# Kernel optimization log

Hardware: AMD Instinct MI355X
Metric: run time of the kernel (lower is better)

Reference implementation:

```python
import jax, jax.numpy as jnp
import numpy as np

C = 256
HEADS = 8
HEAD_DIM = C // HEADS
GROUPS = 8
EPS = 1e-5


def setup_inputs() -> dict:
    key = jax.random.key(0)
    ks = jax.random.split(key, 11)
    B, S = 2, 16
    s = 0.02
    return {
        "x": jax.random.normal(ks[0], (B, C, S, S, S), dtype=jnp.float32),
        "gn_w": jnp.ones((C,), jnp.float32),
        "gn_b": jnp.zeros((C,), jnp.float32),
        "wq": jax.random.normal(ks[1], (C, C), jnp.float32) * s,
        "bq": jnp.zeros((C,), jnp.float32),
        "wk": jax.random.normal(ks[2], (C, C), jnp.float32) * s,
        "bk": jnp.zeros((C,), jnp.float32),
        "wv": jax.random.normal(ks[3], (C, C), jnp.float32) * s,
        "bv": jnp.zeros((C,), jnp.float32),
        "wo": jax.random.normal(ks[4], (C, C), jnp.float32) * s,
        "bo": jnp.zeros((C,), jnp.float32),
    }


def _group_norm(x, w, b):
    # x: [B, C, D, H, W]; GroupNorm(8, C) with affine params
    B, Cc, D, H, W = x.shape
    xg = x.reshape(B, GROUPS, Cc // GROUPS, D, H, W)
    mu = jnp.mean(xg, axis=(2, 3, 4, 5), keepdims=True)
    var = jnp.mean(jnp.square(xg - mu), axis=(2, 3, 4, 5), keepdims=True)
    xn = ((xg - mu) * jax.lax.rsqrt(var + EPS)).reshape(B, Cc, D, H, W)
    return xn * w[None, :, None, None, None] + b[None, :, None, None, None]


def reference(x, gn_w, gn_b, wq, bq, wk, bk, wv, bv, wo, bo):
    B, Cc, D, H, W = x.shape
    N = D * H * W
    xn = _group_norm(x, gn_w, gn_b).reshape(B, Cc, N)  # [B,C,N]
    # 1x1x1 Conv3d == per-voxel linear: weight [out,in]
    Q = jnp.einsum("oc,bcn->bon", wq, xn) + bq[None, :, None]
    K = jnp.einsum("oc,bcn->bon", wk, xn) + bk[None, :, None]
    V = jnp.einsum("oc,bcn->bon", wv, xn) + bv[None, :, None]
    Q = Q.reshape(B, HEADS, HEAD_DIM, N)
    K = K.reshape(B, HEADS, HEAD_DIM, N)
    V = V.reshape(B, HEADS, HEAD_DIM, N)
    scale = np.sqrt(HEAD_DIM).astype(np.float32)
    attn = jnp.einsum("bhdn,bhdm->bhnm", Q, K) / scale
    attn = jax.nn.softmax(attn, axis=-1)
    out = jnp.einsum("bhnm,bhdm->bhdn", attn, V)  # [B,h,hd,N]
    out = out.reshape(B, Cc, N)
    out = jnp.einsum("oc,bcn->bon", wo, out) + bo[None, :, None]
    return x + out.reshape(B, Cc, D, H, W)
```

## Files before the change

### kernel.cpp

```cpp
#include <hip/hip_runtime.h>

#define B_   2
#define C_   256
#define N_   4096
#define H_   8
#define HD_  32
#define G_   8
#define CPG_ 32

typedef short short8 __attribute__((ext_vector_type(8)));
typedef float f32x4  __attribute__((ext_vector_type(4)));
typedef float f4     __attribute__((ext_vector_type(4)));

__device__ __forceinline__ float b2f(short s) {
    return __uint_as_float(((unsigned)(unsigned short)s) << 16);
}
__device__ __forceinline__ short f2b(float f) {
    unsigned u = __float_as_uint(f);
    unsigned r = (u + 0x7FFF + ((u >> 16) & 1)) >> 16;
    return (short)r;
}

__global__ __launch_bounds__(256) void gn_part(const float* __restrict__ x,
                                               float* __restrict__ part) {
    int blk = blockIdx.x;
    const f4* p = (const f4*)x + (size_t)(blk >> 6) * (CPG_ * N_ / 4) + (size_t)(blk & 63) * 512;
    float s = 0.f, ss = 0.f;
#pragma unroll
    for (int i = 0; i < 2; i++) {
        f4 v = p[threadIdx.x + i * 256];
#pragma unroll
        for (int j = 0; j < 4; j++) { float f = v[j]; s += f; ss += f * f; }
    }
#pragma unroll
    for (int off = 32; off > 0; off >>= 1) {
        s  += __shfl_down(s, off);
        ss += __shfl_down(ss, off);
    }
    __shared__ float rs[4], rss[4];
    int w = threadIdx.x >> 6;
    if ((threadIdx.x & 63) == 0) { rs[w] = s; rss[w] = ss; }
    __syncthreads();
    if (threadIdx.x == 0) {
        part[blk * 2]     = rs[0] + rs[1] + rs[2] + rs[3];
        part[blk * 2 + 1] = rss[0] + rss[1] + rss[2] + rss[3];
    }
}

__global__ __launch_bounds__(256) void gemm_qkv(
    const float* __restrict__ x,
    const float* __restrict__ gw, const float* __restrict__ gb,
    const float* __restrict__ part,
    const float* __restrict__ wq, const float* __restrict__ bq,
    const float* __restrict__ wk, const float* __restrict__ bk,
    const float* __restrict__ wv, const float* __restrict__ bv,
    short* __restrict__ q, short* __restrict__ kt, short* __restrict__ v) {
    int z = blockIdx.z;
    int b = z / 3, which = z % 3;
    const float* W    = which == 0 ? wq : (which == 1 ? wk : wv);
    const float* bias = which == 0 ? bq : (which == 1 ? bk : bv);
    bool trans = (which != 2);
    float mul = (which == 0) ? (0.17677669529663687f * 1.4426950408889634f) : 1.0f;

    __shared__ short wl[64][40];
    __shared__ short xl[128][40];
    __shared__ float ga[256], gbb[256];
    __shared__ float mus[8], rstds[8];

    int o0 = blockIdx.y * 64, n0 = blockIdx.x * 128;
    int tid = threadIdx.x;
    int w = tid >> 6, lane = tid & 63, li = lane & 15, quad = lane >> 4;
    int wr = w & 1, wc = w >> 1;

#pragma unroll
    for (int gi = 0; gi < 2; gi++) {
        int g = w * 2 + gi;
        const float* pp = &part[(size_t)(b * 8 + g) * 128 + lane * 2];
        float s = pp[0], ss = pp[1];
#pragma unroll
        for (int off = 32; off > 0; off >>= 1) {
            s  += __shfl_down(s, off);
            ss += __shfl_down(ss, off);
        }
        if (lane == 0) {
            const float inv = 1.f / (float)(CPG_ * N_);
            float mu = s * inv;
            float var = ss * inv - mu * mu;
            mus[g] = mu;
            rstds[g] = rsqrtf(var + 1e-5f);
        }
    }
    __syncthreads();
    {
        int c = tid, g = c >> 5;
        float a = rstds[g] * gw[c];
        ga[c]  = a;
        gbb[c] = gb[c] - mus[g] * a;
    }

    f32x4 acc[8];
#pragma unroll
    for (int i = 0; i < 8; i++) acc[i] = (f32x4){0.f, 0.f, 0.f, 0.f};

    int cpair = tid >> 4, l16 = tid & 15;
    __syncthreads();

    for (int k0 = 0; k0 < 256; k0 += 32) {
        {
            int row = tid >> 2, co = (tid & 3) << 3;
            const float* wp = &W[(size_t)(o0 + row) * 256 + k0 + co];
            f4 wa = *(const f4*)wp;
            f4 wb = *(const f4*)(wp + 4);
            short8 w8;
#pragma unroll
            for (int j = 0; j < 4; j++) { w8[j] = f2b(wa[j]); w8[j + 4] = f2b(wb[j]); }
            *(short8*)&wl[row][co] = w8;
        }
        {
            int c0 = k0 + cpair * 2;
            float a0 = ga[c0],     b0c = gbb[c0];
            float a1 = ga[c0 + 1], b1c = gbb[c0 + 1];
            const float* xr0 = x + ((size_t)(b * 256 + c0)) * N_ + n0 + l16;
            const float* xr1 = xr0 + N_;
#pragma unroll
            for (int j = 0; j < 8; j++) {
                unsigned lo = (unsigned short)f2b(xr0[16 * j] * a0 + b0c);
                unsigned hi = (unsigned short)f2b(xr1[16 * j] * a1 + b1c);
                *(unsigned*)&xl[l16 + 16 * j][cpair * 2] = lo | (hi << 16);
            }
        }
        __syncthreads();
        short8 af[4], bfr[4];
        if (trans) {
#pragma unroll
            for (int i = 0; i < 4; i++) af[i]  = *(short8*)&xl[wr * 64 + i * 16 + li][quad * 8];
#pragma unroll
            for (int j = 0; j < 2; j++) bfr[j] = *(short8*)&wl[wc * 32 + j * 16 + li][quad * 8];
#pragma unroll
            for (int i = 0; i < 4; i++)
#pragma unroll
                for (int j = 0; j < 2; j++)
                    acc[i * 2 + j] = __builtin_amdgcn_mfma_f32_16x16x32_bf16(af[i], bfr[j], acc[i * 2 + j], 0, 0, 0);
        } else {
#pragma unroll
            for (int i = 0; i < 2; i++) af[i]  = *(short8*)&wl[wr * 32 + i * 16 + li][quad * 8];
#pragma unroll
            for (int j = 0; j < 4; j++) bfr[j] = *(short8*)&xl[wc * 64 + j * 16 + li][quad * 8];
#pragma unroll
            for (int i = 0; i < 2; i++)
#pragma unroll
                for (int j = 0; j < 4; j++)
                    acc[i * 4 + j] = __builtin_amdgcn_mfma_f32_16x16x32_bf16(af[i], bfr[j], acc[i * 4 + j], 0, 0, 0);
        }
        __syncthreads();
    }

    if (which == 2) {
        short* outp = v + (size_t)b * C_ * N_;
#pragma unroll
        for (int i = 0; i < 2; i++) {
            int ob = o0 + wr * 32 + i * 16 + quad * 4;
#pragma unroll
            for (int j = 0; j < 4; j++) {
                int n_ = n0 + wc * 64 + j * 16 + li;
#pragma unroll
                for (int r = 0; r < 4; r++) {
                    float val = acc[i * 4 + j][r] + bias[ob + r];
                    outp[(size_t)(ob + r) * N_ + n_] = f2b(val);
                }
            }
        }
    } else if (which == 0) {
        short* outp = q + (size_t)b * N_ * C_;
#pragma unroll
        for (int i = 0; i < 4; i++) {
            int nb_ = n0 + wr * 64 + i * 16 + quad * 4;
#pragma unroll
            for (int j = 0; j < 2; j++) {
                int o_ = o0 + wc * 32 + j * 16 + li;
                float bv_ = bias[o_];
#pragma unroll
                for (int r = 0; r < 4; r++)
                    outp[(size_t)(nb_ + r) * C_ + o_] = f2b((acc[i * 2 + j][r] + bv_) * mul);
            }
        }
    } else {
#pragma unroll
        for (int i = 0; i < 4; i++) {
            int nb_ = n0 + wr * 64 + i * 16 + quad * 4;
#pragma unroll
            for (int j = 0; j < 2; j++) {
                int o_ = o0 + wc * 32 + j * 16 + li;
                int hh = o_ >> 5, d = o_ & 31;
                float bv_ = bias[o_];
                short* kdst = kt + ((size_t)(b * 8 + hh) * N_) * HD_ + d;
#pragma unroll
                for (int r = 0; r < 4; r++)
                    kdst[(size_t)(nb_ + r) * HD_] = f2b(acc[i * 2 + j][r] + bv_);
            }
        }
    }
}

#define STAGE_BARRIER(bufk, bufv)                                         \
    *(short8*)&kl[(bufk) * 2560 + klo] = kst;                             \
    *(short8*)&vl[(bufv) * 2304 + vlo] = vst;                             \
    __syncthreads();

#define PREFETCH(t1)                                                      \
    kst = *(const short8*)(kgp + (size_t)(t1) * 64 * HD_);                \
    vst = *(const short8*)(vgp + (t1) * 64);

#define LOADVF(vf, bufv)                                                  \
    vf[0] = *(short8*)&vl[(bufv) * 2304 + li * 72 + quad * 8];            \
    vf[1] = *(short8*)&vl[(bufv) * 2304 + (16 + li) * 72 + quad * 8];     \
    vf[2] = *(short8*)&vl[(bufv) * 2304 + li * 72 + 32 + quad * 8];       \
    vf[3] = *(short8*)&vl[(bufv) * 2304 + (16 + li) * 72 + 32 + quad * 8];

#define QK(bufk)                                                          \
    _Pragma("unroll")                                                     \
    for (int c = 0; c < 4; c++) {                                         \
        short8 kf = *(short8*)&kl[(bufk) * 2560 + (c * 16 + li) * 40 + quad * 8]; \
        s0[c] = __builtin_amdgcn_mfma_f32_16x16x32_bf16(kf, qf0, zero, 0, 0, 0);  \
        s1[c] = __builtin_amdgcn_mfma_f32_16x16x32_bf16(kf, qf1, zero, 0, 0, 0);  \
    }

#define PV(pP, vf)                                                        \
    {                                                                     \
        short8 pf00 = *(short8*)&(pP)[li * 72 + quad * 8];                \
        short8 pf01 = *(short8*)&(pP)[li * 72 + 32 + quad * 8];           \
        short8 pf10 = *(short8*)&(pP)[1152 + li * 72 + quad * 8];         \
        short8 pf11 = *(short8*)&(pP)[1152 + li * 72 + 32 + quad * 8];    \
        oa00 = __builtin_amdgcn_mfma_f32_16x16x32_bf16(pf00, vf[0], oa00, 0, 0, 0); \
        oa01 = __builtin_amdgcn_mfma_f32_16x16x32_bf16(pf00, vf[1], oa01, 0, 0, 0); \
        oa00 = __builtin_amdgcn_mfma_f32_16x16x32_bf16(pf01, vf[2], oa00, 0, 0, 0); \
        oa01 = __builtin_amdgcn_mfma_f32_16x16x32_bf16(pf01, vf[3], oa01, 0, 0, 0); \
        oa10 = __builtin_amdgcn_mfma_f32_16x16x32_bf16(pf10, vf[0], oa10, 0, 0, 0); \
        oa11 = __builtin_amdgcn_mfma_f32_16x16x32_bf16(pf10, vf[1], oa11, 0, 0, 0); \
        oa10 = __builtin_amdgcn_mfma_f32_16x16x32_bf16(pf11, vf[2], oa10, 0, 0, 0); \
        oa11 = __builtin_amdgcn_mfma_f32_16x16x32_bf16(pf11, vf[3], oa11, 0, 0, 0); \
    }

#define EXPPACK(pC)                                                       \
    {                                                                     \
        float lp = 0.f;                                                   \
        _Pragma("unroll")                                                 \
        for (int c = 0; c < 4; c++) {                                     \
            float e0 = __builtin_amdgcn_exp2f(s0[c][0]);                  \
            float e1 = __builtin_amdgcn_exp2f(s0[c][1]);                  \
            float e2 = __builtin_amdgcn_exp2f(s0[c][2]);                  \
            float e3 = __builtin_amdgcn_exp2f(s0[c][3]);                  \
            lp += (e0 + e1) + (e2 + e3);                                  \
            unsigned pk0 = __builtin_amdgcn_perm(__float_as_uint(e1), __float_as_uint(e0), 0x07060302); \
            unsigned pk1 = __builtin_amdgcn_perm(__float_as_uint(e3), __float_as_uint(e2), 0x07060302); \
            uint2 pkv; pkv.x = pk0; pkv.y = pk1;                          \
            *(uint2*)&(pC)[li * 72 + c * 16 + quad * 4] = pkv;            \
        }                                                                 \
        lr0 += lp;                                                        \
        lp = 0.f;                                                         \
        _Pragma("unroll")                                                 \
        for (int c = 0; c < 4; c++) {                                     \
            float e0 = __builtin_amdgcn_exp2f(s1[c][0]);                  \
            float e1 = __builtin_amdgcn_exp2f(s1[c][1]);                  \
            float e2 = __builtin_amdgcn_exp2f(s1[c][2]);                  \
            float e3 = __builtin_amdgcn_exp2f(s1[c][3]);                  \
            lp += (e0 + e1) + (e2 + e3);                                  \
            unsigned pk0 = __builtin_amdgcn_perm(__float_as_uint(e1), __float_as_uint(e0), 0x07060302); \
            unsigned pk1 = __builtin_amdgcn_perm(__float_as_uint(e3), __float_as_uint(e2), 0x07060302); \
            uint2 pkv; pkv.x = pk0; pkv.y = pk1;                          \
            *(uint2*)&(pC)[1152 + li * 72 + c * 16 + quad * 4] = pkv;     \
        }                                                                 \
        lr1 += lp;                                                        \
    }

__global__ __launch_bounds__(256) void flash(const short* __restrict__ q,
                                             const short* __restrict__ ktp,
                                             const short* __restrict__ v,
                                             short* __restrict__ aoT) {
    int bid = blockIdx.x;
    int xcd = bid & 7;
    int s_  = bid >> 3;
    int bh  = xcd * 2 + (s_ & 1);
    int nb  = s_ >> 1;
    int b = bh >> 3, h = bh & 7;

    const short* QT = q   + (size_t)b * N_ * C_ + h * HD_;
    const short* KP = ktp + (size_t)bh * N_ * HD_;
    const short* V  = v   + ((size_t)b * C_ + h * HD_) * N_;
    short* O = aoT + (size_t)b * N_ * C_ + h * HD_;

    __shared__ short kl[2 * 2560];
    __shared__ short vl[2 * 2304];
    __shared__ short pl[4 * 4608];

    int tid = threadIdx.x, w = tid >> 6, lane = tid & 63, li = lane & 15, quad = lane >> 4;
    int n0w = nb * 128 + w * 32;
    short* pA = pl + w * 4608;
    short* pB = pA + 2304;

    short8 qf0 = *(const short8*)&QT[(size_t)(n0w + li) * 256 + quad * 8];
    short8 qf1 = *(const short8*)&QT[(size_t)(n0w + 16 + li) * 256 + quad * 8];

    f32x4 oa00 = (f32x4){0.f,0.f,0.f,0.f}, oa01 = oa00, oa10 = oa00, oa11 = oa00;
    float lr0 = 0.f, lr1 = 0.f;
    const f32x4 zero = (f32x4){0.f, 0.f, 0.f, 0.f};

    int krow = tid >> 2, kcol = (tid & 3) << 3;
    int vrow = tid >> 3, vcol = (tid & 7) << 3;
    const short* kgp = KP + (size_t)krow * HD_ + kcol;
    const short* vgp = V + (size_t)vrow * N_ + vcol;
    int klo = krow * 40 + kcol;
    int vlo = vrow * 72 + vcol;

    short8 kst = *(const short8*)kgp;
    short8 vst = *(const short8*)vgp;
    short8 vfa[4], vfb[4];
    f32x4 s0[4], s1[4];

    STAGE_BARRIER(0, 0);
    PREFETCH(1);
    LOADVF(vfa, 0);
    QK(0);
    EXPPACK(pA);

    for (int mt = 1; mt < 62; mt += 2) {
        STAGE_BARRIER(1, 1);
        PREFETCH(mt + 1);
        LOADVF(vfb, 1);
        QK(1);
        PV(pA, vfa);
        EXPPACK(pB);
        STAGE_BARRIER(0, 0);
        PREFETCH(mt + 2);
        LOADVF(vfa, 0);
        QK(0);
        PV(pB, vfb);
        EXPPACK(pA);
    }
    STAGE_BARRIER(1, 1);
    LOADVF(vfb, 1);
    QK(1);
    PV(pA, vfa);
    EXPPACK(pB);
    PV(pB, vfb);

    lr0 += __shfl_xor(lr0, 16); lr0 += __shfl_xor(lr0, 32);
    lr1 += __shfl_xor(lr1, 16); lr1 += __shfl_xor(lr1, 32);
#pragma unroll
    for (int r2 = 0; r2 < 4; r2++) {
        float ln0 = __shfl(lr0, quad * 4 + r2);
        float inv0 = 1.f / ln0;
        size_t n_ = (size_t)(n0w + quad * 4 + r2);
        O[n_ * 256 + li]      = f2b(oa00[r2] * inv0);
        O[n_ * 256 + 16 + li] = f2b(oa01[r2] * inv0);
        float ln1 = __shfl(lr1, quad * 4 + r2);
        float inv1 = 1.f / ln1;
        size_t n2 = (size_t)(n0w + 16 + quad * 4 + r2);
        O[n2 * 256 + li]      = f2b(oa10[r2] * inv1);
        O[n2 * 256 + 16 + li] = f2b(oa11[r2] * inv1);
    }
}

__global__ __launch_bounds__(256) void gemm_out(const float* __restrict__ W,
                                                const float* __restrict__ bias,
                                                const short* __restrict__ aoT,
                                                const float* __restrict__ resid,
                                                float* __restrict__ out) {
    int b = blockIdx.z;
    const short* X = aoT + (size_t)b * N_ * C_;
    const float* R = resid + (size_t)b * C_ * N_;
    float* outp = out + (size_t)b * C_ * N_;

    __shared__ short wl[128][40];
    __shared__ short xl[64][40];

    int o0 = blockIdx.y * 128, n0 = blockIdx.x * 64;
    int tid = threadIdx.x;
    int w = tid >> 6, lane = tid & 63, li = lane & 15, quad = lane >> 4;
    int wr = w & 1, wc = w >> 1;

    f32x4 acc[4][2];
#pragma unroll
    for (int i = 0; i < 4; i++)
#pragma unroll
        for (int j = 0; j < 2; j++) acc[i][j] = (f32x4){0.f, 0.f, 0.f, 0.f};

    for (int k0 = 0; k0 < 256; k0 += 32) {
#pragma unroll
        for (int i = 0; i < 2; i++) {
            int idx = tid + i * 256;
            int row = idx >> 2, co = (idx & 3) << 3;
            const float* wp = &W[(size_t)(o0 + row) * 256 + k0 + co];
            f4 wa = *(const f4*)wp;
            f4 wb = *(const f4*)(wp + 4);
            short8 w8;
#pragma unroll
            for (int j = 0; j < 4; j++) { w8[j] = f2b(wa[j]); w8[j + 4] = f2b(wb[j]); }
            *(short8*)&wl[row][co] = w8;
        }
        {
            int row = tid >> 2, co = (tid & 3) << 3;
            *(short8*)&xl[row][co] = *(const short8*)&X[(size_t)(n0 + row) * 256 + k0 + co];
        }
        __syncthreads();
        short8 af[4], bfr[2];
#pragma unroll
        for (int i = 0; i < 4; i++) af[i]  = *(short8*)&wl[wr * 64 + i * 16 + li][quad * 8];
#pragma unroll
        for (int j = 0; j < 2; j++) bfr[j] = *(short8*)&xl[wc * 32 + j * 16 + li][quad * 8];
#pragma unroll
        for (int i = 0; i < 4; i++)
#pragma unroll
            for (int j = 0; j < 2; j++)
                acc[i][j] = __builtin_amdgcn_mfma_f32_16x16x32_bf16(af[i], bfr[j], acc[i][j], 0, 0, 0);
        __syncthreads();
    }
#pragma unroll
    for (int i = 0; i < 4; i++) {
        int ob = o0 + wr * 64 + i * 16 + quad * 4;
#pragma unroll
        for (int j = 0; j < 2; j++) {
            int n_ = n0 + wc * 32 + j * 16 + li;
#pragma unroll
            for (int r = 0; r < 4; r++) {
                size_t idx = (size_t)(ob + r) * N_ + n_;
                outp[idx] = acc[i][j][r] + bias[ob + r] + R[idx];
            }
        }
    }
}

extern "C" void kernel_launch(void* const* d_in, const int* in_sizes, int n_in,
                              void* d_out, int out_size, void* d_ws, size_t ws_size,
                              hipStream_t stream) {
    const float* x  = (const float*)d_in[0];
    const float* gw = (const float*)d_in[1];
    const float* gb = (const float*)d_in[2];
    const float* wq = (const float*)d_in[3];
    const float* bq = (const float*)d_in[4];
    const float* wk = (const float*)d_in[5];
    const float* bk = (const float*)d_in[6];
    const float* wv = (const float*)d_in[7];
    const float* bv = (const float*)d_in[8];
    const float* wo = (const float*)d_in[9];
    const float* bo = (const float*)d_in[10];
    float* out = (float*)d_out;

    char* ws = (char*)d_ws;
    float* part = (float*)ws;
    const size_t TS = (size_t)B_ * N_ * C_;
    short* aoT = (short*)(ws + 16384);
    short* q   = aoT + TS;
    short* kt  = q + TS;
    short* v   = kt + TS;

    gn_part<<<1024, 256, 0, stream>>>(x, part);
    gemm_qkv<<<dim3(32, 4, 6), 256, 0, stream>>>(x, gw, gb, part,
                                                 wq, bq, wk, bk, wv, bv, q, kt, v);
    flash<<<512, 256, 0, stream>>>(q, kt, v, aoT);
    gemm_out<<<dim3(64, 2, 2), 256, 0, stream>>>(wo, bo, aoT, x, out);
}
```

Before: 171.8 us.

## Keep softmax probabilities in registers and use 8 waves of 16 query rows

The flash kernel now runs 8 waves per block, each handling 16 query rows instead of 32. Exponentiated scores are packed straight into MFMA A-operand registers rather than written to and re-read from a shared-memory P buffer. The V tile is loaded with a permuted column order so the register layout of P matches the V fragment layout. It also adds s_setprio around the MFMA blocks and replaces the manually software-pipelined unrolled loop with a simple double-buffered loop. The aim is to remove the LDS round trip for P and raise occupancy, at the cost of more K/V LDS reads per query row and less explicit overlap.

```diff
diff --git a/kernel.cpp b/kernel.cpp
--- a/kernel.cpp
+++ b/kernel.cpp
@@ -9,6 +9,8 @@
 #define CPG_ 32
 
 typedef short short8 __attribute__((ext_vector_type(8)));
+typedef short short4v __attribute__((ext_vector_type(4)));
+typedef unsigned uint4v __attribute__((ext_vector_type(4)));
 typedef float f32x4  __attribute__((ext_vector_type(4)));
 typedef float f4     __attribute__((ext_vector_type(4)));
 
@@ -202,78 +204,7 @@
     }
 }
 
-#define STAGE_BARRIER(bufk, bufv)                                         \
-    *(short8*)&kl[(bufk) * 2560 + klo] = kst;                             \
-    *(short8*)&vl[(bufv) * 2304 + vlo] = vst;                             \
-    __syncthreads();
-
-#define PREFETCH(t1)                                                      \
-    kst = *(const short8*)(kgp + (size_t)(t1) * 64 * HD_);                \
-    vst = *(const short8*)(vgp + (t1) * 64);
-
-#define LOADVF(vf, bufv)                                                  \
-    vf[0] = *(short8*)&vl[(bufv) * 2304 + li * 72 + quad * 8];            \
-    vf[1] = *(short8*)&vl[(bufv) * 2304 + (16 + li) * 72 + quad * 8];     \
-    vf[2] = *(short8*)&vl[(bufv) * 2304 + li * 72 + 32 + quad * 8];       \
-    vf[3] = *(short8*)&vl[(bufv) * 2304 + (16 + li) * 72 + 32 + quad * 8];
-
-#define QK(bufk)                                                          \
-    _Pragma("unroll")                                                     \
-    for (int c = 0; c < 4; c++) {                                         \
-        short8 kf = *(short8*)&kl[(bufk) * 2560 + (c * 16 + li) * 40 + quad * 8]; \
-        s0[c] = __builtin_amdgcn_mfma_f32_16x16x32_bf16(kf, qf0, zero, 0, 0, 0);  \
-        s1[c] = __builtin_amdgcn_mfma_f32_16x16x32_bf16(kf, qf1, zero, 0, 0, 0);  \
-    }
-
-#define PV(pP, vf)                                                        \
-    {                                                                     \
-        short8 pf00 = *(short8*)&(pP)[li * 72 + quad * 8];                \
-        short8 pf01 = *(short8*)&(pP)[li * 72 + 32 + quad * 8];           \
-        short8 pf10 = *(short8*)&(pP)[1152 + li * 72 + quad * 8];         \
-        short8 pf11 = *(short8*)&(pP)[1152 + li * 72 + 32 + quad * 8];    \
-        oa00 = __builtin_amdgcn_mfma_f32_16x16x32_bf16(pf00, vf[0], oa00, 0, 0, 0); \
-        oa01 = __builtin_amdgcn_mfma_f32_16x16x32_bf16(pf00, vf[1], oa01, 0, 0, 0); \
-        oa00 = __builtin_amdgcn_mfma_f32_16x16x32_bf16(pf01, vf[2], oa00, 0, 0, 0); \
-        oa01 = __builtin_amdgcn_mfma_f32_16x16x32_bf16(pf01, vf[3], oa01, 0, 0, 0); \
-        oa10 = __builtin_amdgcn_mfma_f32_16x16x32_bf16(pf10, vf[0], oa10, 0, 0, 0); \
-        oa11 = __builtin_amdgcn_mfma_f32_16x16x32_bf16(pf10, vf[1], oa11, 0, 0, 0); \
-        oa10 = __builtin_amdgcn_mfma_f32_16x16x32_bf16(pf11, vf[2], oa10, 0, 0, 0); \
-        oa11 = __builtin_amdgcn_mfma_f32_16x16x32_bf16(pf11, vf[3], oa11, 0, 0, 0); \
-    }
-
-#define EXPPACK(pC)                                                       \
-    {                                                                     \
-        float lp = 0.f;                                                   \
-        _Pragma("unroll")                                                 \
-        for (int c = 0; c < 4; c++) {                                     \
-            float e0 = __builtin_amdgcn_exp2f(s0[c][0]);                  \
-            float e1 = __builtin_amdgcn_exp2f(s0[c][1]);                  \
-            float e2 = __builtin_amdgcn_exp2f(s0[c][2]);                  \
-            float e3 = __builtin_amdgcn_exp2f(s0[c][3]);                  \
-            lp += (e0 + e1) + (e2 + e3);                                  \
-            unsigned pk0 = __builtin_amdgcn_perm(__float_as_uint(e1), __float_as_uint(e0), 0x07060302); \
-            unsigned pk1 = __builtin_amdgcn_perm(__float_as_uint(e3), __float_as_uint(e2), 0x07060302); \
-            uint2 pkv; pkv.x = pk0; pkv.y = pk1;                          \
-            *(uint2*)&(pC)[li * 72 + c * 16 + quad * 4] = pkv;            \
-        }                                                                 \
-        lr0 += lp;                                                        \
-        lp = 0.f;                                                         \
-        _Pragma("unroll")                                                 \
-        for (int c = 0; c < 4; c++) {                                     \
-            float e0 = __builtin_amdgcn_exp2f(s1[c][0]);                  \
-            float e1 = __builtin_amdgcn_exp2f(s1[c][1]);                  \
-            float e2 = __builtin_amdgcn_exp2f(s1[c][2]);                  \
-            float e3 = __builtin_amdgcn_exp2f(s1[c][3]);                  \
-            lp += (e0 + e1) + (e2 + e3);                                  \
-            unsigned pk0 = __builtin_amdgcn_perm(__float_as_uint(e1), __float_as_uint(e0), 0x07060302); \
-            unsigned pk1 = __builtin_amdgcn_perm(__float_as_uint(e3), __float_as_uint(e2), 0x07060302); \
-            uint2 pkv; pkv.x = pk0; pkv.y = pk1;                          \
-            *(uint2*)&(pC)[1152 + li * 72 + c * 16 + quad * 4] = pkv;     \
-        }                                                                 \
-        lr1 += lp;                                                        \
-    }
-
-__global__ __launch_bounds__(256) void flash(const short* __restrict__ q,
+__global__ __launch_bounds__(512) void flash(const short* __restrict__ q,
                                              const short* __restrict__ ktp,
                                              const short* __restrict__ v,
                                              short* __restrict__ aoT) {
@@ -291,61 +222,80 @@
 
     __shared__ short kl[2 * 2560];
     __shared__ short vl[2 * 2304];
-    __shared__ short pl[4 * 4608];
 
     int tid = threadIdx.x, w = tid >> 6, lane = tid & 63, li = lane & 15, quad = lane >> 4;
-    int n0w = nb * 128 + w * 32;
-    short* pA = pl + w * 4608;
-    short* pB = pA + 2304;
+    int n0w = nb * 128 + w * 16;
 
     short8 qf0 = *(const short8*)&QT[(size_t)(n0w + li) * 256 + quad * 8];
-    short8 qf1 = *(const short8*)&QT[(size_t)(n0w + 16 + li) * 256 + quad * 8];
-
-    f32x4 oa00 = (f32x4){0.f,0.f,0.f,0.f}, oa01 = oa00, oa10 = oa00, oa11 = oa00;
-    float lr0 = 0.f, lr1 = 0.f;
+
+    f32x4 oa00 = (f32x4){0.f,0.f,0.f,0.f}, oa01 = oa00;
+    float lr0 = 0.f;
     const f32x4 zero = (f32x4){0.f, 0.f, 0.f, 0.f};
 
-    int krow = tid >> 2, kcol = (tid & 3) << 3;
-    int vrow = tid >> 3, vcol = (tid & 7) << 3;
+    int krow = tid >> 3, kcol = (tid & 7) << 2;
     const short* kgp = KP + (size_t)krow * HD_ + kcol;
-    const short* vgp = V + (size_t)vrow * N_ + vcol;
     int klo = krow * 40 + kcol;
-    int vlo = vrow * 72 + vcol;
-
-    short8 kst = *(const short8*)kgp;
-    short8 vst = *(const short8*)vgp;
-    short8 vfa[4], vfb[4];
-    f32x4 s0[4], s1[4];
-
-    STAGE_BARRIER(0, 0);
-    PREFETCH(1);
-    LOADVF(vfa, 0);
-    QK(0);
-    EXPPACK(pA);
-
-    for (int mt = 1; mt < 62; mt += 2) {
-        STAGE_BARRIER(1, 1);
-        PREFETCH(mt + 1);
-        LOADVF(vfb, 1);
-        QK(1);
-        PV(pA, vfa);
-        EXPPACK(pB);
-        STAGE_BARRIER(0, 0);
-        PREFETCH(mt + 2);
-        LOADVF(vfa, 0);
-        QK(0);
-        PV(pB, vfb);
-        EXPPACK(pA);
-    }
-    STAGE_BARRIER(1, 1);
-    LOADVF(vfb, 1);
-    QK(1);
-    PV(pA, vfa);
-    EXPPACK(pB);
-    PV(pB, vfb);
+    int vd = tid >> 4, g = tid & 15;
+    int mbase = 32 * (g >> 3) + 16 * (g & 1) + 4 * ((g >> 1) & 3);
+    const short* vgp = V + (size_t)vd * N_ + mbase;
+    int vlo = vd * 72 + g * 4;
+
+    short4v kst = *(const short4v*)kgp;
+    short4v vst = *(const short4v*)vgp;
+
+    f32x4 s0[4];
+    short8 vf[4];
+
+    for (int t = 0; t < 64; ++t) {
+        int buf = t & 1;
+        *(short4v*)&kl[buf * 2560 + klo] = kst;
+        *(short4v*)&vl[buf * 2304 + vlo] = vst;
+        if (t < 63) {
+            kst = *(const short4v*)(kgp + (size_t)(t + 1) * 64 * HD_);
+            vst = *(const short4v*)(vgp + (t + 1) * 64);
+        }
+        __syncthreads();
+
+        __builtin_amdgcn_s_setprio(1);
+#pragma unroll
+        for (int c = 0; c < 4; c++) {
+            short8 kf = *(short8*)&kl[buf * 2560 + (c * 16 + li) * 40 + quad * 8];
+            s0[c] = __builtin_amdgcn_mfma_f32_16x16x32_bf16(kf, qf0, zero, 0, 0, 0);
+        }
+        __builtin_amdgcn_s_setprio(0);
+
+        vf[0] = *(short8*)&vl[buf * 2304 + li * 72 + quad * 8];
+        vf[1] = *(short8*)&vl[buf * 2304 + (16 + li) * 72 + quad * 8];
+        vf[2] = *(short8*)&vl[buf * 2304 + li * 72 + 32 + quad * 8];
+        vf[3] = *(short8*)&vl[buf * 2304 + (16 + li) * 72 + 32 + quad * 8];
+
+        unsigned paw[8];
+        float lp = 0.f;
+#pragma unroll
+        for (int c = 0; c < 4; c++) {
+            float e0 = __builtin_amdgcn_exp2f(s0[c][0]);
+            float e1 = __builtin_amdgcn_exp2f(s0[c][1]);
+            float e2 = __builtin_amdgcn_exp2f(s0[c][2]);
+            float e3 = __builtin_amdgcn_exp2f(s0[c][3]);
+            lp += (e0 + e1) + (e2 + e3);
+            paw[2 * c]     = __builtin_amdgcn_perm(__float_as_uint(e1), __float_as_uint(e0), 0x07060302);
+            paw[2 * c + 1] = __builtin_amdgcn_perm(__float_as_uint(e3), __float_as_uint(e2), 0x07060302);
+        }
+        lr0 += lp;
+        uint4v p0 = (uint4v){paw[0], paw[1], paw[2], paw[3]};
+        uint4v p1 = (uint4v){paw[4], paw[5], paw[6], paw[7]};
+        short8 af0 = __builtin_bit_cast(short8, p0);
+        short8 af1 = __builtin_bit_cast(short8, p1);
+
+        __builtin_amdgcn_s_setprio(1);
+        oa00 = __builtin_amdgcn_mfma_f32_16x16x32_bf16(af0, vf[0], oa00, 0, 0, 0);
+        oa01 = __builtin_amdgcn_mfma_f32_16x16x32_bf16(af0, vf[1], oa01, 0, 0, 0);
+        oa00 = __builtin_amdgcn_mfma_f32_16x16x32_bf16(af1, vf[2], oa00, 0, 0, 0);
+        oa01 = __builtin_amdgcn_mfma_f32_16x16x32_bf16(af1, vf[3], oa01, 0, 0, 0);
+        __builtin_amdgcn_s_setprio(0);
+    }
 
     lr0 += __shfl_xor(lr0, 16); lr0 += __shfl_xor(lr0, 32);
-    lr1 += __shfl_xor(lr1, 16); lr1 += __shfl_xor(lr1, 32);
 #pragma unroll
     for (int r2 = 0; r2 < 4; r2++) {
         float ln0 = __shfl(lr0, quad * 4 + r2);
@@ -353,11 +303,6 @@
         size_t n_ = (size_t)(n0w + quad * 4 + r2);
         O[n_ * 256 + li]      = f2b(oa00[r2] * inv0);
         O[n_ * 256 + 16 + li] = f2b(oa01[r2] * inv0);
-        float ln1 = __shfl(lr1, quad * 4 + r2);
-        float inv1 = 1.f / ln1;
-        size_t n2 = (size_t)(n0w + 16 + quad * 4 + r2);
-        O[n2 * 256 + li]      = f2b(oa10[r2] * inv1);
-        O[n2 * 256 + 16 + li] = f2b(oa11[r2] * inv1);
     }
 }
 
@@ -457,6 +402,6 @@
     gn_part<<<1024, 256, 0, stream>>>(x, part);
     gemm_qkv<<<dim3(32, 4, 6), 256, 0, stream>>>(x, gw, gb, part,
                                                  wq, bq, wk, bk, wv, bv, q, kt, v);
-    flash<<<512, 256, 0, stream>>>(q, kt, v, aoT);
+    flash<<<512, 512, 0, stream>>>(q, kt, v, aoT);
     gemm_out<<<dim3(64, 2, 2), 256, 0, stream>>>(wo, bo, aoT, x, out);
 }
```

Result: faster. 155.5 us (-9.5%).
